# Kernel tuning notes

Hardware: AMD Instinct MI355X
Metric: run time of the kernel (lower is better)

The kernel has to match this reference:

```python
import jax, jax.numpy as jnp
import numpy as np

ALPHA = 10.0  # anchor scale: anchors = eye(C) * ALPHA


def setup_inputs() -> dict:
    key = jax.random.key(0)
    k_x, k_w = jax.random.split(key)
    B, D, C = 16384, 768, 1024
    x = jax.random.normal(k_x, (B, D), dtype=jnp.float32)
    # nn.Linear(input_dim, num_classes, bias=False).weight has shape (C, D)
    W = jax.random.normal(k_w, (C, D), dtype=jnp.float32) * (1.0 / np.sqrt(D))
    return {"x": x, "W": W}


def reference(x, W):
    # logits: (B, C) = x @ W^T
    logits = jnp.einsum("bd,cd->bc", x, W)
    # distances[b, j] = || logits[b] - alpha * e_j ||_2
    # = sqrt(||logits[b]||^2 - 2*alpha*logits[b, j] + alpha^2)
    # (exact algebraic identity for diagonal anchors; avoids the (B, C, C) intermediate)
    sq_norm = jnp.sum(logits * logits, axis=-1, keepdims=True)  # (B, 1)
    d2 = sq_norm - 2.0 * ALPHA * logits + ALPHA * ALPHA          # (B, C)
    distances = jnp.sqrt(jnp.maximum(d2, 0.0))
    return logits, distances
```

## Files before the change

kernel.cpp:

```cpp
#include <hip/hip_runtime.h>
#include <hip/hip_bf16.h>
#include <stdint.h>


#define M_DIM 16384
#define N_DIM 1024
#define K_DIM 768
#define ALPHA_F 10.0f

typedef __bf16 bf16x8 __attribute__((ext_vector_type(8)));
typedef float f32x4 __attribute__((ext_vector_type(4)));

static __device__ __forceinline__ bf16x8 cvt8(f32x4 a, f32x4 b) {
  union { __bf16 h[8]; bf16x8 v; } p;
  p.h[0] = (__bf16)a[0]; p.h[1] = (__bf16)a[1];
  p.h[2] = (__bf16)a[2]; p.h[3] = (__bf16)a[3];
  p.h[4] = (__bf16)b[0]; p.h[5] = (__bf16)b[1];
  p.h[6] = (__bf16)b[2]; p.h[7] = (__bf16)b[3];
  return p.v;
}

__global__ __launch_bounds__(256) void cvt_w_kernel(const float* __restrict__ Wm,
                                                    unsigned short* __restrict__ Wq) {
  int tid = blockIdx.x * 256 + threadIdx.x;
  int l15 = tid & 15;
  int q = (tid >> 4) & 3;
  int mi = (tid >> 6) & 7;
  int rem = tid >> 9;
  int kt = rem % 24;
  int chunk = rem / 24;
  int col = chunk * 128 + mi * 16 + l15;
  int k = kt * 32 + q * 8;
  const f32x4* p = (const f32x4*)(Wm + (size_t)col * K_DIM + k);
  *(bf16x8*)(Wq + (size_t)tid * 8) = cvt8(p[0], p[1]);
}

__global__ __launch_bounds__(1024, 4) void fused_kernel(
    const float* __restrict__ X,
    const unsigned short* __restrict__ Wq,
    float* __restrict__ logits,
    float* __restrict__ dist) {
  __shared__ __align__(16) unsigned short xt[64 * 768];
  __shared__ float rs[64][16];

  const int t = threadIdx.x;
  const int lane = t & 63;
  const int w = t >> 6;
  const int q = lane >> 4;
  const int l15 = lane & 15;

  const int bid = blockIdx.x;
  const int tm = (bid & 7) * 32 + (bid >> 3);

  const float* Xb = X + (size_t)tm * 64 * K_DIM;

#pragma unroll
  for (int r = 0; r < 6; ++r) {
    int id = r * 1024 + t;
    int row = id / 96;
    int c = id - row * 96;
    const f32x4* g = (const f32x4*)(Xb + (size_t)row * K_DIM + c * 8);
    f32x4 a = g[0], b = g[1];
    *(bf16x8*)(&xt[row * 768 + (c ^ (row & 7)) * 8]) = cvt8(a, b);
  }
  __syncthreads();

  f32x4 acc[4][4] = {};
  float part[4] = {};
  const unsigned short* wchunk =
      Wq + ((size_t)((w >> 1) * 24) * 512 + (w & 1) * 256 + lane) * 8;
  const float a2 = ALPHA_F * ALPHA_F;
  float* Lb = logits + (size_t)tm * 64 * N_DIM + w * 64 + q * 4;
  float* Db = dist + (size_t)tm * 64 * N_DIM + w * 64 + q * 4;

#pragma unroll
  for (int p = 0; p < 2; ++p) {
#pragma unroll 2
    for (int kt = 0; kt < 24; ++kt) {
      bf16x8 bx[4];
#pragma unroll
      for (int ni = 0; ni < 4; ++ni) {
        int row = ni * 16 + l15;
        bx[ni] = *(const bf16x8*)(&xt[row * 768 + ((kt * 4 + q) ^ (row & 7)) * 8]);
      }
      const unsigned short* wp = wchunk + (size_t)kt * 512 * 8;
      bf16x8 af[2];
#pragma unroll
      for (int j = 0; j < 2; ++j) af[j] = *(const bf16x8*)(wp + (p * 2 + j) * 512);
#pragma unroll
      for (int j = 0; j < 2; ++j)
#pragma unroll
        for (int ni = 0; ni < 4; ++ni)
          acc[p * 2 + j][ni] = __builtin_amdgcn_mfma_f32_16x16x32_bf16(
              af[j], bx[ni], acc[p * 2 + j][ni], 0, 0, 0);
    }
#pragma unroll
    for (int ni = 0; ni < 4; ++ni) {
      size_t roff = (size_t)(ni * 16 + l15) * N_DIM;
#pragma unroll
      for (int j = 0; j < 2; ++j) {
        f32x4 lv = acc[p * 2 + j][ni];
        *(f32x4*)(Lb + roff + (p * 2 + j) * 16) = lv;
#pragma unroll
        for (int k = 0; k < 4; ++k) part[ni] += lv[k] * lv[k];
      }
    }
  }

#pragma unroll
  for (int m = 16; m <= 32; m <<= 1)
#pragma unroll
    for (int ni = 0; ni < 4; ++ni) part[ni] += __shfl_xor(part[ni], m, 64);
  if (q == 0) {
#pragma unroll
    for (int ni = 0; ni < 4; ++ni) rs[ni * 16 + l15][w] = part[ni];
  }
  __syncthreads();

  float S[4];
#pragma unroll
  for (int ni = 0; ni < 4; ++ni) {
    const float* rp = &rs[ni * 16 + l15][0];
    f32x4 a = *(const f32x4*)(rp + 0);
    f32x4 b = *(const f32x4*)(rp + 4);
    f32x4 c = *(const f32x4*)(rp + 8);
    f32x4 d = *(const f32x4*)(rp + 12);
    S[ni] = ((a[0] + a[1] + a[2] + a[3]) + (b[0] + b[1] + b[2] + b[3])) +
            ((c[0] + c[1] + c[2] + c[3]) + (d[0] + d[1] + d[2] + d[3]));
  }

#pragma unroll
  for (int ni = 0; ni < 4; ++ni) {
    size_t roff = (size_t)(ni * 16 + l15) * N_DIM;
#pragma unroll
    for (int mi = 0; mi < 4; ++mi) {
      f32x4 lv = acc[mi][ni];
      f32x4 d;
#pragma unroll
      for (int j = 0; j < 4; ++j)
        d[j] = sqrtf(fmaxf(S[ni] - 2.0f * ALPHA_F * lv[j] + a2, 0.0f));
      *(f32x4*)(Db + roff + mi * 16) = d;
    }
  }
}

extern "C" void kernel_launch(void* const* d_in, const int* in_sizes, int n_in,
                              void* d_out, int out_size, void* d_ws, size_t ws_size,
                              hipStream_t stream) {
  const float* x = (const float*)d_in[0];
  const float* W = (const float*)d_in[1];
  float* logits = (float*)d_out;
  float* dist = logits + (size_t)M_DIM * N_DIM;

  unsigned short* Wq = (unsigned short*)d_ws;

  cvt_w_kernel<<<(N_DIM * K_DIM / 8) / 256, 256, 0, stream>>>(W, Wq);
  fused_kernel<<<M_DIM / 64, 1024, 0, stream>>>(x, Wq, logits, dist);
}
```

Measured before the change: 57.15 us.

## Overlap second half of X tile staging with first-half MFMA k-steps; nontemporal stores

```diff
diff --git a/kernel.cpp b/kernel.cpp
--- a/kernel.cpp
+++ b/kernel.cpp
@@ -55,10 +55,10 @@
   const float* Xb = X + (size_t)tm * 64 * K_DIM;
 
 #pragma unroll
-  for (int r = 0; r < 6; ++r) {
+  for (int r = 0; r < 3; ++r) {
     int id = r * 1024 + t;
-    int row = id / 96;
-    int c = id - row * 96;
+    int row = id / 48;
+    int c = id - row * 48;
     const f32x4* g = (const f32x4*)(Xb + (size_t)row * K_DIM + c * 8);
     f32x4 a = g[0], b = g[1];
     *(bf16x8*)(&xt[row * 768 + (c ^ (row & 7)) * 8]) = cvt8(a, b);
@@ -73,39 +73,58 @@
   float* Lb = logits + (size_t)tm * 64 * N_DIM + w * 64 + q * 4;
   float* Db = dist + (size_t)tm * 64 * N_DIM + w * 64 + q * 4;
 
+  auto kstep = [&](int kt, int mi0) {
+    bf16x8 bx[4];
 #pragma unroll
-  for (int p = 0; p < 2; ++p) {
-#pragma unroll 2
-    for (int kt = 0; kt < 24; ++kt) {
-      bf16x8 bx[4];
+    for (int ni = 0; ni < 4; ++ni) {
+      int row = ni * 16 + l15;
+      bx[ni] = *(const bf16x8*)(&xt[row * 768 + ((kt * 4 + q) ^ (row & 7)) * 8]);
+    }
+    const unsigned short* wp = wchunk + (size_t)kt * 512 * 8;
+    bf16x8 af0 = *(const bf16x8*)(wp + mi0 * 512);
+    bf16x8 af1 = *(const bf16x8*)(wp + (mi0 + 1) * 512);
 #pragma unroll
-      for (int ni = 0; ni < 4; ++ni) {
-        int row = ni * 16 + l15;
-        bx[ni] = *(const bf16x8*)(&xt[row * 768 + ((kt * 4 + q) ^ (row & 7)) * 8]);
-      }
-      const unsigned short* wp = wchunk + (size_t)kt * 512 * 8;
-      bf16x8 af[2];
+    for (int ni = 0; ni < 4; ++ni)
+      acc[mi0][ni] = __builtin_amdgcn_mfma_f32_16x16x32_bf16(af0, bx[ni], acc[mi0][ni], 0, 0, 0);
 #pragma unroll
-      for (int j = 0; j < 2; ++j) af[j] = *(const bf16x8*)(wp + (p * 2 + j) * 512);
-#pragma unroll
-      for (int j = 0; j < 2; ++j)
-#pragma unroll
-        for (int ni = 0; ni < 4; ++ni)
-          acc[p * 2 + j][ni] = __builtin_amdgcn_mfma_f32_16x16x32_bf16(
-              af[j], bx[ni], acc[p * 2 + j][ni], 0, 0, 0);
-    }
+    for (int ni = 0; ni < 4; ++ni)
+      acc[mi0 + 1][ni] = __builtin_amdgcn_mfma_f32_16x16x32_bf16(af1, bx[ni], acc[mi0 + 1][ni], 0, 0, 0);
+  };
+
+  auto store_pass = [&](int p) {
 #pragma unroll
     for (int ni = 0; ni < 4; ++ni) {
       size_t roff = (size_t)(ni * 16 + l15) * N_DIM;
 #pragma unroll
       for (int j = 0; j < 2; ++j) {
         f32x4 lv = acc[p * 2 + j][ni];
-        *(f32x4*)(Lb + roff + (p * 2 + j) * 16) = lv;
+        __builtin_nontemporal_store(lv, (f32x4*)(Lb + roff + (p * 2 + j) * 16));
 #pragma unroll
         for (int k = 0; k < 4; ++k) part[ni] += lv[k] * lv[k];
       }
     }
+  };
+
+#pragma unroll 2
+  for (int kt = 0; kt < 12; ++kt) {
+    if (kt < 3) {
+      int id = kt * 1024 + t;
+      int row = id / 48;
+      int cx = id - row * 48;
+      int c = 48 + cx;
+      const f32x4* g = (const f32x4*)(Xb + (size_t)row * K_DIM + c * 8);
+      f32x4 a = g[0], b = g[1];
+      *(bf16x8*)(&xt[row * 768 + (c ^ (row & 7)) * 8]) = cvt8(a, b);
+    }
+    kstep(kt, 0);
   }
+  __syncthreads();
+#pragma unroll 2
+  for (int kt = 12; kt < 24; ++kt) kstep(kt, 0);
+  store_pass(0);
+#pragma unroll 2
+  for (int kt = 0; kt < 24; ++kt) kstep(kt, 2);
+  store_pass(1);
 
 #pragma unroll
   for (int m = 16; m <= 32; m <<= 1)
@@ -139,7 +158,7 @@
 #pragma unroll
       for (int j = 0; j < 4; ++j)
         d[j] = sqrtf(fmaxf(S[ni] - 2.0f * ALPHA_F * lv[j] + a2, 0.0f));
-      *(f32x4*)(Db + roff + mi * 16) = d;
+      __builtin_nontemporal_store(d, (f32x4*)(Db + roff + mi * 16));
     }
   }
 }
```

New measurement: 65.64 us. 1.15x slower.
